# Performance work log

Measured on AMD Instinct MI355X. Metric: run time of the kernel, lower is better.

## Reference

```python
import jax, jax.numpy as jnp
import numpy as np

B, A, D, H = 16384, 16, 512, 512


def setup_inputs() -> dict:
    key = jax.random.key(0)
    ks = jax.random.split(key, 8)
    s = 1.0 / np.sqrt(D)
    sh = 1.0 / np.sqrt(H)
    return {
        "state": jax.random.normal(ks[0], (B, D), jnp.float32),
        "W1": jax.random.normal(ks[1], (A, D, H), jnp.float32) * s,
        "b1": jax.random.normal(ks[2], (A, H), jnp.float32) * s,
        "W2": jax.random.normal(ks[3], (A, H, H), jnp.float32) * sh,
        "b2": jax.random.normal(ks[4], (A, H), jnp.float32) * sh,
        "W3": jax.random.normal(ks[5], (A, H, 1), jnp.float32) * sh,
        "b3": jax.random.normal(ks[6], (A, 1), jnp.float32) * sh,
        "actions": jax.random.randint(ks[7], (B,), 0, A, jnp.int64),
    }


def reference(state, W1, b1, W2, b2, W3, b3, actions):
    # All per-action MLPs applied to every state as grouped/batched GEMMs.
    # h1, h2: [B, A, H]; out: [B, A, n_out]
    h1 = jax.nn.relu(jnp.einsum("bd,adh->bah", state, W1) + b1)
    h2 = jax.nn.relu(jnp.einsum("bah,ahk->bak", h1, W2) + b2)
    out = jnp.einsum("bah,ahk->bak", h2, W3) + b3  # [B, A, 1]
    # Gather the selected action's output per batch element -> [B, n_out]
    return jnp.take_along_axis(out, actions[:, None, None], axis=1)[:, 0, :]
```

## Files before the change

### kernel.cpp

```cpp
#include <hip/hip_runtime.h>
#include <hip/hip_bf16.h>
#include <stdint.h>

typedef __hip_bfloat16 bf16;
typedef float f32x4 __attribute__((ext_vector_type(4)));
typedef short bf16x8 __attribute__((ext_vector_type(8)));

#define NB 16384
#define NA 16
#define ND 512
#define NH 512
#define TR 80

#define W1S_OFF 0u
#define W2S_OFF 8388608u
#define PERM_OFF 16777216u
#define META_OFF 16842752u

__device__ __forceinline__ unsigned short f2b(float x) {
  unsigned int b = __float_as_uint(x);
  return (unsigned short)((b + 0x7FFFu + ((b >> 16) & 1u)) >> 16);
}

__global__ __launch_bounds__(256) void k_prep(const float* __restrict__ W1,
                                              const float* __restrict__ W2,
                                              bf16* __restrict__ W1s,
                                              bf16* __restrict__ W2s,
                                              const int* __restrict__ act,
                                              int* __restrict__ meta,
                                              int* __restrict__ perm) {
  if (blockIdx.x == 2048) {
    __shared__ int hist[16][256];
    __shared__ int off16[16];
    int t = threadIdx.x;
    int lane = t & 63, wv = t >> 6;
#pragma unroll
    for (int i = 0; i < 16; ++i) hist[i][t] = 0;
    __syncthreads();
    for (int j = 0; j < 64; ++j) {
      int a = act[t + (j << 8)] & 15;
      hist[a][t]++;
    }
    __syncthreads();
    for (int q = 0; q < 4; ++q) {
      int a = (wv << 2) + q;
      int base = lane << 2;
      int v0 = hist[a][base + 0];
      int v1 = hist[a][base + 1];
      int v2 = hist[a][base + 2];
      int v3 = hist[a][base + 3];
      int s = v0 + v1 + v2 + v3;
      int incl = s;
#pragma unroll
      for (int d = 1; d < 64; d <<= 1) {
        int y = __shfl_up(incl, d);
        if (lane >= d) incl += y;
      }
      int excl = incl - s;
      hist[a][base + 0] = excl;
      hist[a][base + 1] = excl + v0;
      hist[a][base + 2] = excl + v0 + v1;
      hist[a][base + 3] = excl + v0 + v1 + v2;
      if (lane == 63) off16[a] = incl;
    }
    __syncthreads();
    if (t == 0) {
      int o = 0;
      for (int aa = 0; aa < 16; ++aa) {
        int c = off16[aa];
        meta[aa] = c;
        meta[16 + aa] = o;
        off16[aa] = o;
        o += c;
      }
    }
    __syncthreads();
    for (int j = 0; j < 64; ++j) {
      int idx = t + (j << 8);
      int a = act[idx] & 15;
      int pos = off16[a] + hist[a][t]++;
      perm[pos] = idx;
    }
    return;
  }
  __shared__ float tile[64][65];
  int blk = blockIdx.x;
  int m = blk >> 6;
  int tl = blk & 63;
  int td = tl >> 3, th = tl & 7;
  const float* src = (m < NA) ? (W1 + (size_t)m * (ND * NH)) : (W2 + (size_t)(m - NA) * (ND * NH));
  char* dstb = (m < NA) ? ((char*)W1s + ((size_t)m << 19)) : ((char*)W2s + ((size_t)(m - NA) << 19));
  int t = threadIdx.x;
  int r = t >> 2, c0 = (t & 3) << 4;
  const float* sp = src + (size_t)(td * 64 + r) * NH + th * 64 + c0;
  float4 v0 = ((const float4*)sp)[0];
  float4 v1 = ((const float4*)sp)[1];
  float4 v2 = ((const float4*)sp)[2];
  float4 v3 = ((const float4*)sp)[3];
  float* tr = &tile[r][c0];
  tr[0] = v0.x; tr[1] = v0.y; tr[2] = v0.z; tr[3] = v0.w;
  tr[4] = v1.x; tr[5] = v1.y; tr[6] = v1.z; tr[7] = v1.w;
  tr[8] = v2.x; tr[9] = v2.y; tr[10] = v2.z; tr[11] = v2.w;
  tr[12] = v3.x; tr[13] = v3.y; tr[14] = v3.z; tr[15] = v3.w;
  __syncthreads();
  int wv = t >> 6, l = t & 63;
  int l15b = l & 15, l4b = l >> 4;
#pragma unroll
  for (int kc = 0; kc < 2; ++kc) {
    union { unsigned short us[8]; uint4 q; } u;
#pragma unroll
    for (int i = 0; i < 8; ++i)
      u.us[i] = f2b(tile[kc * 32 + l4b * 8 + i][wv * 16 + l15b]);
    int hb = th * 4 + wv;
    int kb = td * 2 + kc;
    *(uint4*)(dstb + ((size_t)(hb * 16 + kb) << 10) + (l << 4)) = u.q;
  }
}

__global__ __launch_bounds__(1024) void k_main(
    const float* __restrict__ state, const float* __restrict__ b1,
    const float* __restrict__ b2, const float* __restrict__ W3,
    const float* __restrict__ b3, const bf16* __restrict__ W1s,
    const bf16* __restrict__ W2s, const int* __restrict__ perm,
    const int* __restrict__ meta, float* __restrict__ out) {
  extern __shared__ char smem[];
  char* Xs = smem;
  float* outbuf = (float*)(smem + 81920);

  int bid = blockIdx.x;
  int xcd = bid & 7, slot = bid >> 3;
  int a0 = xcd << 1;
  int n0 = meta[a0], n1 = meta[a0 + 1];
  int nt0 = (n0 + TR - 1) / TR, nt1 = (n1 + TR - 1) / TR;
  int a, t;
  if (slot < nt0) {
    a = a0; t = slot;
  } else if (slot < nt0 + nt1) {
    a = a0 + 1; t = slot - nt0;
  } else {
    return;
  }
  int rowbase = meta[16 + a] + t * TR;
  int nrows = meta[a] - t * TR;
  nrows = nrows > TR ? TR : nrows;

  int tid = threadIdx.x;
  int lane = tid & 63;
  int w = tid >> 6;
  int l15 = lane & 15, l4 = lane >> 4;

  const char* Wl = (const char*)W1s + ((size_t)a << 19) + (w << 15) + (lane << 4);
  const char* Wl2 = (const char*)W2s + ((size_t)a << 19) + (w << 15) + (lane << 4);

  bf16x8 A[2][2];
  bf16x8 Bc[5], Bn[5];
#pragma unroll
  for (int s = 0; s < 2; ++s)
#pragma unroll
    for (int hf = 0; hf < 2; ++hf)
      A[s][hf] = *(const bf16x8*)(Wl + (hf << 14) + (s << 10));

  {
#pragma unroll
    for (int it = 0; it < 10; ++it) {
      int c = tid + (it << 10);
      int row = c >> 7, chunk = c & 127;
      int gr = (row < nrows) ? perm[rowbase + row] : -1;
      float4 v = make_float4(0.f, 0.f, 0.f, 0.f);
      if (gr >= 0) v = *(const float4*)(state + (size_t)gr * ND + (chunk << 2));
      uint2 pk;
      pk.x = (unsigned)f2b(v.x) | ((unsigned)f2b(v.y) << 16);
      pk.y = (unsigned)f2b(v.z) | ((unsigned)f2b(v.w) << 16);
      *(uint2*)(Xs + row * 1024 + ((chunk << 3) ^ ((row & 7) << 4))) = pk;
    }
  }
  __syncthreads();

  uint2 h1p[10];

  {
    f32x4 acc[2][5] = {};
#pragma unroll
    for (int bf = 0; bf < 5; ++bf) {
      int b = (bf << 4) + l15;
      Bc[bf] = *(const bf16x8*)(Xs + b * 1024 + ((l4 << 4) ^ ((b & 7) << 4)));
    }
#pragma unroll
    for (int ks = 0; ks < 16; ++ks) {
      if (ks < 15) {
#pragma unroll
        for (int bf = 0; bf < 5; ++bf) {
          int b = (bf << 4) + l15;
          Bn[bf] = *(const bf16x8*)(Xs + b * 1024 + ((((ks + 1) << 6) + (l4 << 4)) ^ ((b & 7) << 4)));
        }
      }
#pragma unroll
      for (int hf = 0; hf < 2; ++hf)
#pragma unroll
        for (int bf = 0; bf < 5; ++bf)
          acc[hf][bf] = __builtin_amdgcn_mfma_f32_16x16x32_bf16(A[ks & 1][hf], Bc[bf], acc[hf][bf], 0, 0, 0);
      if (ks < 14) {
#pragma unroll
        for (int hf = 0; hf < 2; ++hf)
          A[ks & 1][hf] = *(const bf16x8*)(Wl + (hf << 14) + ((ks + 2) << 10));
      }
#pragma unroll
      for (int bf = 0; bf < 5; ++bf) Bc[bf] = Bn[bf];
    }
#pragma unroll
    for (int s = 0; s < 2; ++s)
#pragma unroll
      for (int hf = 0; hf < 2; ++hf)
        A[s][hf] = *(const bf16x8*)(Wl2 + (hf << 14) + (s << 10));
#pragma unroll
    for (int hf = 0; hf < 2; ++hf) {
      int hb = (w << 5) + (hf << 4) + (l4 << 2);
      float4 bias = *(const float4*)(b1 + (a << 9) + hb);
#pragma unroll
      for (int bf = 0; bf < 5; ++bf) {
        float x0 = fmaxf(acc[hf][bf][0] + bias.x, 0.f);
        float x1 = fmaxf(acc[hf][bf][1] + bias.y, 0.f);
        float x2 = fmaxf(acc[hf][bf][2] + bias.z, 0.f);
        float x3 = fmaxf(acc[hf][bf][3] + bias.w, 0.f);
        h1p[hf * 5 + bf].x = (unsigned)f2b(x0) | ((unsigned)f2b(x1) << 16);
        h1p[hf * 5 + bf].y = (unsigned)f2b(x2) | ((unsigned)f2b(x3) << 16);
      }
    }
  }
  __syncthreads();
#pragma unroll
  for (int hf = 0; hf < 2; ++hf) {
    int hb2 = ((w << 5) + (hf << 4) + (l4 << 2)) << 1;
#pragma unroll
    for (int bf = 0; bf < 5; ++bf) {
      int b = (bf << 4) + l15;
      *(uint2*)(Xs + b * 1024 + (hb2 ^ ((b & 7) << 4))) = h1p[hf * 5 + bf];
    }
  }
  __syncthreads();

  {
    f32x4 acc[2][5] = {};
#pragma unroll
    for (int bf = 0; bf < 5; ++bf) {
      int b = (bf << 4) + l15;
      Bc[bf] = *(const bf16x8*)(Xs + b * 1024 + ((l4 << 4) ^ ((b & 7) << 4)));
    }
#pragma unroll
    for (int ks = 0; ks < 16; ++ks) {
      if (ks < 15) {
#pragma unroll
        for (int bf = 0; bf < 5; ++bf) {
          int b = (bf << 4) + l15;
          Bn[bf] = *(const bf16x8*)(Xs + b * 1024 + ((((ks + 1) << 6) + (l4 << 4)) ^ ((b & 7) << 4)));
        }
      }
#pragma unroll
      for (int hf = 0; hf < 2; ++hf)
#pragma unroll
        for (int bf = 0; bf < 5; ++bf)
          acc[hf][bf] = __builtin_amdgcn_mfma_f32_16x16x32_bf16(A[ks & 1][hf], Bc[bf], acc[hf][bf], 0, 0, 0);
      if (ks < 14) {
#pragma unroll
        for (int hf = 0; hf < 2; ++hf)
          A[ks & 1][hf] = *(const bf16x8*)(Wl2 + (hf << 14) + ((ks + 2) << 10));
      }
#pragma unroll
      for (int bf = 0; bf < 5; ++bf) Bc[bf] = Bn[bf];
    }
    float part[5] = {0.f, 0.f, 0.f, 0.f, 0.f};
#pragma unroll
    for (int hf = 0; hf < 2; ++hf) {
      int hb = (w << 5) + (hf << 4) + (l4 << 2);
      float4 bias = *(const float4*)(b2 + (a << 9) + hb);
      float4 w3v = *(const float4*)(W3 + (a << 9) + hb);
#pragma unroll
      for (int bf = 0; bf < 5; ++bf) {
        part[bf] += fmaxf(acc[hf][bf][0] + bias.x, 0.f) * w3v.x +
                    fmaxf(acc[hf][bf][1] + bias.y, 0.f) * w3v.y +
                    fmaxf(acc[hf][bf][2] + bias.z, 0.f) * w3v.z +
                    fmaxf(acc[hf][bf][3] + bias.w, 0.f) * w3v.w;
      }
    }
#pragma unroll
    for (int bf = 0; bf < 5; ++bf) {
      float p = part[bf];
      p += __shfl_xor(p, 16);
      p += __shfl_xor(p, 32);
      if (l4 == 0) outbuf[w * TR + (bf << 4) + l15] = p;
    }
  }
  __syncthreads();
  if (tid < nrows) {
    float s = b3[a];
#pragma unroll
    for (int ww = 0; ww < 16; ++ww) s += outbuf[ww * TR + tid];
    out[perm[rowbase + tid]] = s;
  }
}

extern "C" void kernel_launch(void* const* d_in, const int* in_sizes, int n_in,
                              void* d_out, int out_size, void* d_ws, size_t ws_size,
                              hipStream_t stream) {
  const float* state = (const float*)d_in[0];
  const float* W1 = (const float*)d_in[1];
  const float* b1 = (const float*)d_in[2];
  const float* W2 = (const float*)d_in[3];
  const float* b2 = (const float*)d_in[4];
  const float* W3 = (const float*)d_in[5];
  const float* b3 = (const float*)d_in[6];
  const int* actions = (const int*)d_in[7];
  float* out = (float*)d_out;
  char* ws = (char*)d_ws;
  bf16* W1s = (bf16*)(ws + W1S_OFF);
  bf16* W2s = (bf16*)(ws + W2S_OFF);
  int* perm = (int*)(ws + PERM_OFF);
  int* meta = (int*)(ws + META_OFF);

  k_prep<<<2049, 256, 0, stream>>>(W1, W2, W1s, W2s, actions, meta, perm);
  hipFuncSetAttribute((const void*)k_main, hipFuncAttributeMaxDynamicSharedMemorySize, 87040);
  k_main<<<256, 1024, 87040, stream>>>(state, b1, b2, W3, b3, W1s, W2s, perm, meta, out);
}
```

Measured before the change: 50.72 us.

## Fuse weight prep and action sort into main kernel with spin-wait flags

```diff
diff --git a/kernel.cpp b/kernel.cpp
--- a/kernel.cpp
+++ b/kernel.cpp
@@ -22,49 +22,64 @@
   return (unsigned short)((b + 0x7FFFu + ((b >> 16) & 1u)) >> 16);
 }
 
-__global__ __launch_bounds__(256) void k_prep(const float* __restrict__ W1,
-                                              const float* __restrict__ W2,
-                                              bf16* __restrict__ W1s,
-                                              bf16* __restrict__ W2s,
-                                              const int* __restrict__ act,
-                                              int* __restrict__ meta,
-                                              int* __restrict__ perm) {
-  if (blockIdx.x == 2048) {
-    __shared__ int hist[16][256];
-    __shared__ int off16[16];
-    int t = threadIdx.x;
+__global__ __launch_bounds__(1024, 4) void k_fused(
+    const float* __restrict__ state, const float* __restrict__ W1,
+    const float* __restrict__ b1, const float* __restrict__ W2,
+    const float* __restrict__ b2, const float* __restrict__ W3,
+    const float* __restrict__ b3, const int* __restrict__ act,
+    bf16* __restrict__ W1s, bf16* __restrict__ W2s,
+    int* __restrict__ perm, int* __restrict__ meta, float* __restrict__ out) {
+  extern __shared__ char smem[];
+  char* Xs = smem;
+  float* outbuf = (float*)(smem + 81920);
+
+  int bid = blockIdx.x;
+  int tid = threadIdx.x;
+  int xcd = bid & 7, slot = bid >> 3;
+
+  if (bid == 0) {
+    int* hist = (int*)Xs;
+    int* off16 = (int*)(Xs + 16384);
+    int t = tid & 255;
+    bool mt = tid < 256;
     int lane = t & 63, wv = t >> 6;
-#pragma unroll
-    for (int i = 0; i < 16; ++i) hist[i][t] = 0;
-    __syncthreads();
-    for (int j = 0; j < 64; ++j) {
-      int a = act[t + (j << 8)] & 15;
-      hist[a][t]++;
-    }
-    __syncthreads();
-    for (int q = 0; q < 4; ++q) {
-      int a = (wv << 2) + q;
-      int base = lane << 2;
-      int v0 = hist[a][base + 0];
-      int v1 = hist[a][base + 1];
-      int v2 = hist[a][base + 2];
-      int v3 = hist[a][base + 3];
-      int s = v0 + v1 + v2 + v3;
-      int incl = s;
-#pragma unroll
-      for (int d = 1; d < 64; d <<= 1) {
-        int y = __shfl_up(incl, d);
-        if (lane >= d) incl += y;
-      }
-      int excl = incl - s;
-      hist[a][base + 0] = excl;
-      hist[a][base + 1] = excl + v0;
-      hist[a][base + 2] = excl + v0 + v1;
-      hist[a][base + 3] = excl + v0 + v1 + v2;
-      if (lane == 63) off16[a] = incl;
-    }
-    __syncthreads();
-    if (t == 0) {
+    if (mt) {
+#pragma unroll
+      for (int i = 0; i < 16; ++i) hist[i * 256 + t] = 0;
+    }
+    __syncthreads();
+    if (mt) {
+      for (int j = 0; j < 64; ++j) {
+        int a = act[t + (j << 8)] & 15;
+        hist[a * 256 + t]++;
+      }
+    }
+    __syncthreads();
+    if (mt) {
+      for (int q = 0; q < 4; ++q) {
+        int a = (wv << 2) + q;
+        int base = lane << 2;
+        int v0 = hist[a * 256 + base + 0];
+        int v1 = hist[a * 256 + base + 1];
+        int v2 = hist[a * 256 + base + 2];
+        int v3 = hist[a * 256 + base + 3];
+        int s = v0 + v1 + v2 + v3;
+        int incl = s;
+#pragma unroll
+        for (int d = 1; d < 64; d <<= 1) {
+          int y = __shfl_up(incl, d);
+          if (lane >= d) incl += y;
+        }
+        int excl = incl - s;
+        hist[a * 256 + base + 0] = excl;
+        hist[a * 256 + base + 1] = excl + v0;
+        hist[a * 256 + base + 2] = excl + v0 + v1;
+        hist[a * 256 + base + 3] = excl + v0 + v1 + v2;
+        if (lane == 63) off16[a] = incl;
+      }
+    }
+    __syncthreads();
+    if (tid == 0) {
       int o = 0;
       for (int aa = 0; aa < 16; ++aa) {
         int c = off16[aa];
@@ -75,60 +90,85 @@
       }
     }
     __syncthreads();
-    for (int j = 0; j < 64; ++j) {
-      int idx = t + (j << 8);
-      int a = act[idx] & 15;
-      int pos = off16[a] + hist[a][t]++;
-      perm[pos] = idx;
-    }
-    return;
-  }
-  __shared__ float tile[64][65];
-  int blk = blockIdx.x;
-  int m = blk >> 6;
-  int tl = blk & 63;
-  int td = tl >> 3, th = tl & 7;
-  const float* src = (m < NA) ? (W1 + (size_t)m * (ND * NH)) : (W2 + (size_t)(m - NA) * (ND * NH));
-  char* dstb = (m < NA) ? ((char*)W1s + ((size_t)m << 19)) : ((char*)W2s + ((size_t)(m - NA) << 19));
-  int t = threadIdx.x;
-  int r = t >> 2, c0 = (t & 3) << 4;
-  const float* sp = src + (size_t)(td * 64 + r) * NH + th * 64 + c0;
-  float4 v0 = ((const float4*)sp)[0];
-  float4 v1 = ((const float4*)sp)[1];
-  float4 v2 = ((const float4*)sp)[2];
-  float4 v3 = ((const float4*)sp)[3];
-  float* tr = &tile[r][c0];
-  tr[0] = v0.x; tr[1] = v0.y; tr[2] = v0.z; tr[3] = v0.w;
-  tr[4] = v1.x; tr[5] = v1.y; tr[6] = v1.z; tr[7] = v1.w;
-  tr[8] = v2.x; tr[9] = v2.y; tr[10] = v2.z; tr[11] = v2.w;
-  tr[12] = v3.x; tr[13] = v3.y; tr[14] = v3.z; tr[15] = v3.w;
-  __syncthreads();
-  int wv = t >> 6, l = t & 63;
-  int l15b = l & 15, l4b = l >> 4;
-#pragma unroll
-  for (int kc = 0; kc < 2; ++kc) {
-    union { unsigned short us[8]; uint4 q; } u;
-#pragma unroll
-    for (int i = 0; i < 8; ++i)
-      u.us[i] = f2b(tile[kc * 32 + l4b * 8 + i][wv * 16 + l15b]);
-    int hb = th * 4 + wv;
-    int kb = td * 2 + kc;
-    *(uint4*)(dstb + ((size_t)(hb * 16 + kb) << 10) + (l << 4)) = u.q;
-  }
-}
-
-__global__ __launch_bounds__(1024) void k_main(
-    const float* __restrict__ state, const float* __restrict__ b1,
-    const float* __restrict__ b2, const float* __restrict__ W3,
-    const float* __restrict__ b3, const bf16* __restrict__ W1s,
-    const bf16* __restrict__ W2s, const int* __restrict__ perm,
-    const int* __restrict__ meta, float* __restrict__ out) {
-  extern __shared__ char smem[];
-  char* Xs = smem;
-  float* outbuf = (float*)(smem + 81920);
-
-  int bid = blockIdx.x;
-  int xcd = bid & 7, slot = bid >> 3;
+    if (mt) {
+      for (int j = 0; j < 64; ++j) {
+        int idx = t + (j << 8);
+        int a = act[idx] & 15;
+        int pos = off16[a] + hist[a * 256 + t]++;
+        perm[pos] = idx;
+      }
+    }
+    __syncthreads();
+    if (tid == 0) {
+      __threadfence();
+      atomicAdd(&meta[32], 1);
+    }
+  } else {
+    int grp = tid >> 8, t2 = tid & 255;
+    float* tile = (float*)(Xs + grp * 16640);
+    int c = slot - 1;
+    int rounds = (xcd != 0) ? 2 : 3;
+    for (int r = 0; r < rounds; ++r) {
+      int m = grp + (r << 2);
+      int j = (xcd != 0) ? (slot + (m << 5)) : (c + 31 * m);
+      bool valid = (xcd != 0) ? true : (j < 256);
+      int mi = j >> 6;
+      int mat = (mi < 2) ? ((xcd << 1) + mi) : (NA + (xcd << 1) + (mi - 2));
+      const float* src = (mat < NA) ? (W1 + (size_t)mat * (ND * NH))
+                                    : (W2 + (size_t)(mat - NA) * (ND * NH));
+      char* dstb = (mat < NA) ? ((char*)W1s + ((size_t)mat << 19))
+                              : ((char*)W2s + ((size_t)(mat - NA) << 19));
+      int tl = j & 63;
+      int td = tl >> 3, th = tl & 7;
+      if (valid) {
+        int rr = t2 >> 2, c0 = (t2 & 3) << 4;
+        const float* sp = src + (size_t)(td * 64 + rr) * NH + th * 64 + c0;
+        float4 v0 = ((const float4*)sp)[0];
+        float4 v1 = ((const float4*)sp)[1];
+        float4 v2 = ((const float4*)sp)[2];
+        float4 v3 = ((const float4*)sp)[3];
+        float* trp = &tile[rr * 65 + c0];
+        trp[0] = v0.x; trp[1] = v0.y; trp[2] = v0.z; trp[3] = v0.w;
+        trp[4] = v1.x; trp[5] = v1.y; trp[6] = v1.z; trp[7] = v1.w;
+        trp[8] = v2.x; trp[9] = v2.y; trp[10] = v2.z; trp[11] = v2.w;
+        trp[12] = v3.x; trp[13] = v3.y; trp[14] = v3.z; trp[15] = v3.w;
+      }
+      __syncthreads();
+      if (valid) {
+        int wv = t2 >> 6, l = t2 & 63;
+        int l15b = l & 15, l4b = l >> 4;
+#pragma unroll
+        for (int kc = 0; kc < 2; ++kc) {
+          union { unsigned short us[8]; uint4 q; } u;
+#pragma unroll
+          for (int i = 0; i < 8; ++i)
+            u.us[i] = f2b(tile[(kc * 32 + l4b * 8 + i) * 65 + wv * 16 + l15b]);
+          int hb = th * 4 + wv;
+          int kb = td * 2 + kc;
+          *(uint4*)(dstb + ((size_t)(hb * 16 + kb) << 10) + (l << 4)) = u.q;
+        }
+      }
+      __syncthreads();
+    }
+    if (tid == 0) {
+      int nj;
+      if (xcd != 0) {
+        nj = 8;
+      } else {
+        nj = 0;
+        for (int m = 0; m < 12; ++m) nj += (c + 31 * m < 256) ? 1 : 0;
+      }
+      __threadfence();
+      atomicAdd(&meta[33 + xcd], nj);
+    }
+  }
+
+  if (tid == 0) {
+    while (__hip_atomic_load(&meta[32], __ATOMIC_RELAXED, __HIP_MEMORY_SCOPE_AGENT) < 1) {}
+  }
+  __syncthreads();
+  __threadfence();
+
   int a0 = xcd << 1;
   int n0 = meta[a0], n1 = meta[a0 + 1];
   int nt0 = (n0 + TR - 1) / TR, nt1 = (n1 + TR - 1) / TR;
@@ -144,22 +184,11 @@
   int nrows = meta[a] - t * TR;
   nrows = nrows > TR ? TR : nrows;
 
-  int tid = threadIdx.x;
   int lane = tid & 63;
   int w = tid >> 6;
   int l15 = lane & 15, l4 = lane >> 4;
 
-  const char* Wl = (const char*)W1s + ((size_t)a << 19) + (w << 15) + (lane << 4);
-  const char* Wl2 = (const char*)W2s + ((size_t)a << 19) + (w << 15) + (lane << 4);
-
-  bf16x8 A[2][2];
-  bf16x8 Bc[5], Bn[5];
-#pragma unroll
-  for (int s = 0; s < 2; ++s)
-#pragma unroll
-    for (int hf = 0; hf < 2; ++hf)
-      A[s][hf] = *(const bf16x8*)(Wl + (hf << 14) + (s << 10));
-
+  __syncthreads();
   {
 #pragma unroll
     for (int it = 0; it < 10; ++it) {
@@ -174,7 +203,23 @@
       *(uint2*)(Xs + row * 1024 + ((chunk << 3) ^ ((row & 7) << 4))) = pk;
     }
   }
-  __syncthreads();
+
+  if (tid == 0) {
+    while (__hip_atomic_load(&meta[33 + xcd], __ATOMIC_RELAXED, __HIP_MEMORY_SCOPE_AGENT) < 256) {}
+  }
+  __syncthreads();
+  __threadfence();
+
+  const char* Wl = (const char*)W1s + ((size_t)a << 19) + (w << 15) + (lane << 4);
+  const char* Wl2 = (const char*)W2s + ((size_t)a << 19) + (w << 15) + (lane << 4);
+
+  bf16x8 A[2][2];
+  bf16x8 Bc[5], Bn[5];
+#pragma unroll
+  for (int s = 0; s < 2; ++s)
+#pragma unroll
+    for (int hf = 0; hf < 2; ++hf)
+      A[s][hf] = *(const bf16x8*)(Wl + (hf << 14) + (s << 10));
 
   uint2 h1p[10];
 
@@ -317,7 +362,8 @@
   int* perm = (int*)(ws + PERM_OFF);
   int* meta = (int*)(ws + META_OFF);
 
-  k_prep<<<2049, 256, 0, stream>>>(W1, W2, W1s, W2s, actions, meta, perm);
-  hipFuncSetAttribute((const void*)k_main, hipFuncAttributeMaxDynamicSharedMemorySize, 87040);
-  k_main<<<256, 1024, 87040, stream>>>(state, b1, b2, W3, b3, W1s, W2s, perm, meta, out);
+  hipMemsetAsync(meta, 0, 48 * sizeof(int), stream);
+  hipFuncSetAttribute((const void*)k_fused, hipFuncAttributeMaxDynamicSharedMemorySize, 87040);
+  k_fused<<<256, 1024, 87040, stream>>>(state, W1, b1, W2, b2, W3, b3, actions,
+                                        W1s, W2s, perm, meta, out);
 }
```

Result: slower. 196.8 us (+287.9%).
